# Performance work log

Hardware: AMD Instinct MI355X
Metric: run time of the kernel (lower is better)

## Reference

```python
import jax, jax.numpy as jnp
import numpy as np

ROWS = 256
COLS = 256
EPS = 1e-8


def _radius_bins(rows, cols):
    # Same construction as SpectralLoss.__init__: integer radius per rfft bin,
    # ifftshifted along the row axis to match torch.rfft layout.
    shift_rows = rows // 2
    cols_onesided = cols // 2 + 1
    idx = np.indices((rows, cols_onesided)) - np.array([[[shift_rows]], [[0]]])
    r = np.sqrt(idx[0] ** 2 + idx[1] ** 2).astype(int)
    r = np.fft.ifftshift(r, axes=0)
    return r  # [rows, cols_onesided], values in [0, r_max]


def setup_inputs() -> dict:
    key = jax.random.key(0)
    k1, k2 = jax.random.split(key)
    r = _radius_bins(ROWS, COLS)
    vector_length = int(r.max()) + 1  # 182
    data = jax.random.normal(k1, (128, 3, ROWS, COLS), dtype=jnp.float32)
    mean = jax.random.uniform(k2, (vector_length,), dtype=jnp.float32)
    radius = jnp.asarray(r, dtype=jnp.int32)
    return {"data": data, "mean": mean, "radius": radius}


def reference(data, mean, radius):
    L = mean.shape[0]  # vector_length = r_max + 1
    # RGB -> luma (as in SpectralLoss.fft)
    gray = 0.299 * data[:, 0] + 0.587 * data[:, 1] + 0.114 * data[:, 2]  # [B,H,W]
    f = jnp.fft.rfft2(gray)  # [B, H, W//2+1]
    power = f.real ** 2 + f.imag ** 2  # sum of squared re/im parts
    fft_abs = 20.0 * jnp.log(power + EPS)  # [B, H, Wc]
    # Radial histogram: segment-mean keyed on integer radius (replaces the
    # original dense one-hot mask broadcast of shape [B, L, H, Wc]).
    seg = radius.reshape(-1)  # [N] with N = H*Wc
    B = fft_abs.shape[0]
    flat = fft_abs.reshape(B, -1).T  # [N, B]
    sums = jax.ops.segment_sum(flat, seg, num_segments=L)  # [L, B]
    counts = jax.ops.segment_sum(jnp.ones_like(flat[:, :1]), seg, num_segments=L)  # [L, 1]
    profile = (sums / counts).T  # [B, L]
    # Per-sample min-max normalization (same order of ops as torch code)
    profile = profile - jnp.min(profile, axis=1, keepdims=True)
    profile = profile / jnp.max(profile, axis=1, keepdims=True)
    # L1 loss with reduction='sum' against the target mean profile
    return jnp.sum(jnp.abs(profile - mean[None, :]))
```

## Files before the change

kernel.cpp:

```cpp
#include <hip/hip_runtime.h>
#include <cmath>

#define B_   128
#define H_   256
#define W_   256
#define WC_  129
#define L_   182
#define PI_F 3.14159265358979f

__device__ __forceinline__ void fft256_wave(float vr[4], float vi[4], int l) {
  float c0, s0;
  __sincosf(-2.f * PI_F * (float)l / 256.f, &s0, &c0);
  {
    float ur = vr[0] + vr[2], ui = vi[0] + vi[2];
    float dr = vr[0] - vr[2], di = vi[0] - vi[2];
    vr[0] = ur; vi[0] = ui;
    vr[2] = dr * c0 - di * s0; vi[2] = dr * s0 + di * c0;
    float c1 = s0, s1 = -c0;
    ur = vr[1] + vr[3]; ui = vi[1] + vi[3];
    dr = vr[1] - vr[3]; di = vi[1] - vi[3];
    vr[1] = ur; vi[1] = ui;
    vr[3] = dr * c1 - di * s1; vi[3] = dr * s1 + di * c1;
  }
  {
    float c2 = c0 * c0 - s0 * s0, s2 = 2.f * c0 * s0;
    float ur = vr[0] + vr[1], ui = vi[0] + vi[1];
    float dr = vr[0] - vr[1], di = vi[0] - vi[1];
    vr[0] = ur; vi[0] = ui;
    vr[1] = dr * c2 - di * s2; vi[1] = dr * s2 + di * c2;
    ur = vr[2] + vr[3]; ui = vi[2] + vi[3];
    dr = vr[2] - vr[3]; di = vi[2] - vi[3];
    vr[2] = ur; vi[2] = ui;
    vr[3] = dr * c2 - di * s2; vi[3] = dr * s2 + di * c2;
  }
  #pragma unroll
  for (int h = 32; h >= 1; h >>= 1) {
    int i = l & (h - 1);
    float c, s;
    __sincosf(-PI_F * (float)i / (float)h, &s, &c);
    bool up = (l & h) != 0;
    float cc = up ? c : 1.f;
    float ss = up ? s : 0.f;
    float sgn = up ? -1.f : 1.f;
    #pragma unroll
    for (int j = 0; j < 4; ++j) {
      float br = __shfl_xor(vr[j], h, 64);
      float bi = __shfl_xor(vi[j], h, 64);
      float tr = fmaf(sgn, vr[j], br);
      float ti = fmaf(sgn, vi[j], bi);
      vr[j] = tr * cc - ti * ss;
      vi[j] = tr * ss + ti * cc;
    }
  }
}

#define P1_ROWS 16
#define P1_STRIDE 259

__global__ __launch_bounds__(1024) void pass1_kernel(
    const float* __restrict__ data, float2* __restrict__ inter) {
  __shared__ float2 tile[P1_ROWS * P1_STRIDE];
  int tid = threadIdx.x;
  int w = tid >> 6, l = tid & 63;
  int b = blockIdx.x >> 4;
  int row0 = (blockIdx.x & 15) * P1_ROWS;
  int row = row0 + w;
  const float* p0 = data + ((size_t)b * 3) * (H_ * W_) + (size_t)row * W_;
  float vr[4], vi[4];
  #pragma unroll
  for (int j = 0; j < 4; ++j) {
    int i = l + 64 * j;
    float r = p0[i], g = p0[H_ * W_ + i], bl = p0[2 * H_ * W_ + i];
    vr[j] = fmaf(0.299f, r, fmaf(0.587f, g, 0.114f * bl));
    vi[j] = 0.f;
  }
  fft256_wave(vr, vi, l);
  #pragma unroll
  for (int j = 0; j < 4; ++j)
    tile[w * P1_STRIDE + l + 64 * j] = make_float2(vr[j], vi[j]);
  __syncthreads();
  for (int f = tid; f < WC_ * P1_ROWS; f += 1024) {
    int k = f >> 4;
    int r = f & 15;
    int q = (int)(__brev((unsigned)k) >> 24);
    inter[((size_t)b * WC_ + k) * H_ + row0 + r] = tile[r * P1_STRIDE + q];
  }
}

__global__ __launch_bounds__(256) void pass2_kernel(
    const float2* __restrict__ inter, const int* __restrict__ radius,
    float* __restrict__ bins) {
  __shared__ float lbins[L_];
  int tid = threadIdx.x;
  int wv = tid >> 6, l = tid & 63;
  int b = blockIdx.x / 33;
  int g = blockIdx.x - b * 33;
  int k = g * 4 + wv;
  for (int i = tid; i < L_; i += 256) lbins[i] = 0.f;
  __syncthreads();
  if (k < WC_) {
    const float2* p = inter + ((size_t)b * WC_ + k) * H_;
    float vr[4], vi[4];
    #pragma unroll
    for (int j = 0; j < 4; ++j) {
      float2 v = p[l + 64 * j];
      vr[j] = v.x; vi[j] = v.y;
    }
    fft256_wave(vr, vi, l);
    int rb = 4 * (int)(__brev((unsigned)l) >> 26);
    #pragma unroll
    for (int j = 0; j < 4; ++j) {
      int rf = rb + ((j == 1) ? 2 : (j == 2) ? 1 : j);
      float pw = vr[j] * vr[j] + vi[j] * vi[j];
      float val = 20.f * __logf(pw + 1e-8f);
      atomicAdd(&lbins[radius[rf * WC_ + k]], val);
    }
  }
  __syncthreads();
  float* bb = bins + (size_t)b * L_;
  for (int i = tid; i < L_; i += 256) atomicAdd(&bb[i], lbins[i]);
}

__global__ __launch_bounds__(256) void count_kernel(
    const int* __restrict__ radius, float* __restrict__ counts) {
  __shared__ float c[L_];
  int t = threadIdx.x;
  for (int i = t; i < L_; i += 256) c[i] = 0.f;
  __syncthreads();
  for (int i = blockIdx.x * 256 + t; i < H_ * WC_; i += gridDim.x * 256)
    atomicAdd(&c[radius[i]], 1.f);
  __syncthreads();
  for (int i = t; i < L_; i += 256) atomicAdd(&counts[i], c[i]);
}

__global__ __launch_bounds__(256) void loss_kernel(
    const float* __restrict__ bins, const float* __restrict__ counts,
    const float* __restrict__ mean, float* __restrict__ out) {
  int b = blockIdx.x;
  int t = threadIdx.x;
  __shared__ float prof[L_];
  __shared__ float red[256];
  if (t < L_) prof[t] = bins[(size_t)b * L_ + t] / counts[t];
  __syncthreads();
  red[t] = (t < L_) ? prof[t] : INFINITY;
  __syncthreads();
  for (int s = 128; s > 0; s >>= 1) {
    if (t < s) red[t] = fminf(red[t], red[t + s]);
    __syncthreads();
  }
  float mn = red[0];
  __syncthreads();
  red[t] = (t < L_) ? (prof[t] - mn) : -INFINITY;
  __syncthreads();
  for (int s = 128; s > 0; s >>= 1) {
    if (t < s) red[t] = fmaxf(red[t], red[t + s]);
    __syncthreads();
  }
  float mx = red[0];
  __syncthreads();
  red[t] = (t < L_) ? fabsf((prof[t] - mn) / mx - mean[t]) : 0.f;
  __syncthreads();
  for (int s = 128; s > 0; s >>= 1) {
    if (t < s) red[t] += red[t + s];
    __syncthreads();
  }
  if (t == 0) atomicAdd(out, red[0]);
}

extern "C" void kernel_launch(void* const* d_in, const int* in_sizes, int n_in,
                              void* d_out, int out_size, void* d_ws, size_t ws_size,
                              hipStream_t stream) {
  const float* data   = (const float*)d_in[0];
  const float* mean   = (const float*)d_in[1];
  const int*   radius = (const int*)d_in[2];
  float* out = (float*)d_out;

  float2* inter = (float2*)d_ws;
  size_t inter_bytes = (size_t)B_ * WC_ * H_ * sizeof(float2);
  float* bins   = (float*)((char*)d_ws + inter_bytes);
  float* counts = bins + (size_t)B_ * L_;

  hipMemsetAsync(bins, 0, ((size_t)B_ * L_ + L_) * sizeof(float), stream);
  hipMemsetAsync(out, 0, sizeof(float), stream);

  count_kernel<<<64, 256, 0, stream>>>(radius, counts);
  pass1_kernel<<<B_ * 16, 1024, 0, stream>>>(data, inter);
  pass2_kernel<<<B_ * 33, 256, 0, stream>>>(inter, radius, bins);
  loss_kernel<<<B_, 256, 0, stream>>>(bins, counts, mean, out);
}
```

Measured before the change: 200.2 us.

## Replace global atomics and memsets with per-group partials and a final reduction kernel

pass2 now writes per-block partial bin sums to a buffer instead of doing global atomicAdd into per-sample bins, so the memsets are no longer needed. The loss kernel sums the 33 partials per sample and computes the radius counts itself in shared memory, which removes the separate count kernel. A small final kernel reduces the 128 per-sample losses instead of using an atomic on the output. This removes two memset launches and one kernel launch, plus global atomic traffic, but adds a launch and makes every loss block recount all 33k radius entries.

```diff
diff --git a/kernel.cpp b/kernel.cpp
--- a/kernel.cpp
+++ b/kernel.cpp
@@ -6,6 +6,7 @@
 #define W_   256
 #define WC_  129
 #define L_   182
+#define NG_  33
 #define PI_F 3.14159265358979f
 
 __device__ __forceinline__ void fft256_wave(float vr[4], float vi[4], int l) {
@@ -89,12 +90,12 @@
 
 __global__ __launch_bounds__(256) void pass2_kernel(
     const float2* __restrict__ inter, const int* __restrict__ radius,
-    float* __restrict__ bins) {
+    float* __restrict__ partial) {
   __shared__ float lbins[L_];
   int tid = threadIdx.x;
   int wv = tid >> 6, l = tid & 63;
-  int b = blockIdx.x / 33;
-  int g = blockIdx.x - b * 33;
+  int b = blockIdx.x / NG_;
+  int g = blockIdx.x - b * NG_;
   int k = g * 4 + wv;
   for (int i = tid; i < L_; i += 256) lbins[i] = 0.f;
   __syncthreads();
@@ -117,30 +118,29 @@
     }
   }
   __syncthreads();
-  float* bb = bins + (size_t)b * L_;
-  for (int i = tid; i < L_; i += 256) atomicAdd(&bb[i], lbins[i]);
-}
-
-__global__ __launch_bounds__(256) void count_kernel(
-    const int* __restrict__ radius, float* __restrict__ counts) {
-  __shared__ float c[L_];
-  int t = threadIdx.x;
-  for (int i = t; i < L_; i += 256) c[i] = 0.f;
-  __syncthreads();
-  for (int i = blockIdx.x * 256 + t; i < H_ * WC_; i += gridDim.x * 256)
-    atomicAdd(&c[radius[i]], 1.f);
-  __syncthreads();
-  for (int i = t; i < L_; i += 256) atomicAdd(&counts[i], c[i]);
+  float* pp = partial + ((size_t)b * NG_ + g) * L_;
+  for (int i = tid; i < L_; i += 256) pp[i] = lbins[i];
 }
 
 __global__ __launch_bounds__(256) void loss_kernel(
-    const float* __restrict__ bins, const float* __restrict__ counts,
-    const float* __restrict__ mean, float* __restrict__ out) {
+    const float* __restrict__ partial, const int* __restrict__ radius,
+    const float* __restrict__ mean, float* __restrict__ lpart) {
   int b = blockIdx.x;
   int t = threadIdx.x;
+  __shared__ float cnt[L_];
   __shared__ float prof[L_];
   __shared__ float red[256];
-  if (t < L_) prof[t] = bins[(size_t)b * L_ + t] / counts[t];
+  for (int i = t; i < L_; i += 256) cnt[i] = 0.f;
+  __syncthreads();
+  for (int i = t; i < H_ * WC_; i += 256) atomicAdd(&cnt[radius[i]], 1.f);
+  float acc = 0.f;
+  if (t < L_) {
+    const float* pb = partial + (size_t)b * NG_ * L_;
+    #pragma unroll 3
+    for (int g = 0; g < NG_; ++g) acc += pb[g * L_ + t];
+  }
+  __syncthreads();
+  if (t < L_) prof[t] = acc / cnt[t];
   __syncthreads();
   red[t] = (t < L_) ? prof[t] : INFINITY;
   __syncthreads();
@@ -164,7 +164,16 @@
     if (t < s) red[t] += red[t + s];
     __syncthreads();
   }
-  if (t == 0) atomicAdd(out, red[0]);
+  if (t == 0) lpart[b] = red[0];
+}
+
+__global__ __launch_bounds__(64) void final_kernel(
+    const float* __restrict__ lpart, float* __restrict__ out) {
+  int l = threadIdx.x;
+  float v = lpart[l] + lpart[l + 64];
+  #pragma unroll
+  for (int h = 32; h >= 1; h >>= 1) v += __shfl_xor(v, h, 64);
+  if (l == 0) out[0] = v;
 }
 
 extern "C" void kernel_launch(void* const* d_in, const int* in_sizes, int n_in,
@@ -177,14 +186,11 @@
 
   float2* inter = (float2*)d_ws;
   size_t inter_bytes = (size_t)B_ * WC_ * H_ * sizeof(float2);
-  float* bins   = (float*)((char*)d_ws + inter_bytes);
-  float* counts = bins + (size_t)B_ * L_;
+  float* partial = (float*)((char*)d_ws + inter_bytes);
+  float* lpart   = partial + (size_t)B_ * NG_ * L_;
 
-  hipMemsetAsync(bins, 0, ((size_t)B_ * L_ + L_) * sizeof(float), stream);
-  hipMemsetAsync(out, 0, sizeof(float), stream);
-
-  count_kernel<<<64, 256, 0, stream>>>(radius, counts);
   pass1_kernel<<<B_ * 16, 1024, 0, stream>>>(data, inter);
-  pass2_kernel<<<B_ * 33, 256, 0, stream>>>(inter, radius, bins);
-  loss_kernel<<<B_, 256, 0, stream>>>(bins, counts, mean, out);
+  pass2_kernel<<<B_ * NG_, 256, 0, stream>>>(inter, radius, partial);
+  loss_kernel<<<B_, 256, 0, stream>>>(partial, radius, mean, lpart);
+  final_kernel<<<1, 64, 0, stream>>>(lpart, out);
 }
```

Result: slower. 241.2 us (+20.4%).
